# Performance work log

Hardware: AMD Instinct MI355X
Metric: run time of the kernel (lower is better)

The kernel has to match this reference:

```python
import jax, jax.numpy as jnp
import numpy as np

NEG_SLOPE = 0.2  # neg_slope init kwarg


def _segment_softmax(logits, seg, n):
    # numerically stable softmax over edges grouped by destination node
    m = jax.ops.segment_max(logits, seg, num_segments=n)          # [N,H]
    e = jnp.exp(logits - m[seg])                                   # [E,H]
    s = jax.ops.segment_sum(e, seg, num_segments=n)                # [N,H]
    return e / (s[seg] + 1e-16)


def _gat_conv(x, src, dst, W, att_src, att_dst, b, n):
    # PyG GATConv (add_self_loops already applied to src/dst), dropout off (eval)
    H, C = att_src.shape
    h = (x @ W).reshape(n, H, C)                                   # [N,H,C]
    a_src = jnp.einsum('nhc,hc->nh', h, att_src)                   # [N,H]
    a_dst = jnp.einsum('nhc,hc->nh', h, att_dst)                   # [N,H]
    logits = jax.nn.leaky_relu(a_src[src] + a_dst[dst], NEG_SLOPE)  # [E,H]
    alpha = _segment_softmax(logits, dst, n)                       # [E,H]
    msg = h[src] * alpha[:, :, None]                               # [E,H,C]
    out = jax.ops.segment_sum(msg, dst, num_segments=n)            # [N,H,C]
    return out.reshape(n, H * C) + b


def setup_inputs() -> dict:
    key = jax.random.key(0)
    ks = jax.random.split(key, 11)
    NU, NI = 10000, 100000
    N = NU + NI
    E = 1_000_000
    IN, HID, HEADS, OUT = 64, 64, 4, 64
    s = 0.1
    return {
        'edge_index': jax.random.randint(ks[0], (2, E), 0, N, dtype=jnp.int64)
            if jax.config.jax_enable_x64 else jax.random.randint(ks[0], (2, E), 0, N),
        'emb_user': jax.random.normal(ks[1], (NU, IN), jnp.float32) * s,
        'emb_item': jax.random.normal(ks[2], (NI, IN), jnp.float32) * s,
        'W1': jax.random.normal(ks[3], (IN, HEADS * HID), jnp.float32) * s,
        'att_src1': jax.random.normal(ks[4], (HEADS, HID), jnp.float32) * s,
        'att_dst1': jax.random.normal(ks[5], (HEADS, HID), jnp.float32) * s,
        'b1': jnp.zeros((HEADS * HID,), jnp.float32),
        'W2': jax.random.normal(ks[6], (HEADS * HID, OUT), jnp.float32) * s,
        'att_src2': jax.random.normal(ks[7], (1, OUT), jnp.float32) * s,
        'att_dst2': jax.random.normal(ks[8], (1, OUT), jnp.float32) * s,
        'b2': jnp.zeros((OUT,), jnp.float32),
    }


def reference(edge_index, emb_user, emb_item, W1, att_src1, att_dst1, b1,
              W2, att_src2, att_dst2, b2):
    NU = emb_user.shape[0]
    N = NU + emb_item.shape[0]
    x = jnp.concatenate([emb_user, emb_item], axis=0)              # [N,IN]
    # GATConv adds self-loops by default
    loops = jnp.arange(N, dtype=edge_index.dtype)
    src = jnp.concatenate([edge_index[0], loops])
    dst = jnp.concatenate([edge_index[1], loops])
    # dropout layers are identity in eval mode
    x = _gat_conv(x, src, dst, W1, att_src1, att_dst1, b1, N)      # [N,HEADS*HID]
    x = jax.nn.elu(x)
    x = _gat_conv(x, src, dst, W2, att_src2, att_dst2, b2, N)      # [N,OUT]
    return x[:NU], x[NU:]
```

## Files before the change

### kernel.cpp

```cpp
#include <hip/hip_runtime.h>
#include <math.h>


typedef float f32x4 __attribute__((ext_vector_type(4)));
typedef short s16x8 __attribute__((ext_vector_type(8)));

#define CHUNK 2048
#define CAPB 6400
#define PADM 1536
#define CAPT (CAPB + PADM)
#define G2PAD 264
#define SMASK 131071

static __device__ __forceinline__ short f2bf(float f) {
    unsigned u = __builtin_bit_cast(unsigned, f);
    u = (u + 0x7fff + ((u >> 16) & 1)) >> 16;
    return (short)u;
}
static __device__ __forceinline__ float bf2f(unsigned short u) {
    unsigned v = ((unsigned)u) << 16;
    return __builtin_bit_cast(float, v);
}


__global__ __launch_bounds__(256) void bin_kernel(
    const int* __restrict__ ei, int E, int ET, int* __restrict__ acur,
    unsigned long long* __restrict__ staging) {
    __shared__ int cnt[256], delta[256], cur[256];
    int t = threadIdx.x;
    cnt[t] = 0;
    __syncthreads();
    int c0 = blockIdx.x * CHUNK;
    int cend = min(c0 + CHUNK, ET);
    for (int e = c0 + t; e < cend; e += 256) {
        int d = (e < E) ? ei[E + e] : (e - E);
        atomicAdd(&cnt[d >> 9], 1);
    }
    __syncthreads();
    if (t < 64) {
        int loc[4], run = 0;
#pragma unroll
        for (int j = 0; j < 4; ++j) { int v = cnt[t * 4 + j]; loc[j] = run; run += v; }
        int inc = run;
#pragma unroll
        for (int off = 1; off < 64; off <<= 1) {
            int u = __shfl_up(inc, off);
            if (t >= off) inc += u;
        }
        int excl = inc - run;
#pragma unroll
        for (int j = 0; j < 4; ++j) {
            int b = t * 4 + j;
            int lofs = excl + loc[j];
            int c = cnt[b];
            int g = (c > 0) ? atomicAdd(&acur[b], c) : 0;
            delta[b] = b * CAPB + g - lofs;
            cur[b] = lofs;
        }
    }
    __syncthreads();
    for (int e = c0 + t; e < cend; e += 256) {
        int s, d;
        if (e < E) { s = ei[e]; d = ei[E + e]; } else { s = e - E; d = e - E; }
        unsigned long long v = ((unsigned long long)(unsigned)d << 32) | (unsigned)s;
        int b = d >> 9;
        int p = atomicAdd(&cur[b], 1);
        int idx = delta[b] + p;
        if (idx < (b + 1) * CAPB) staging[idx] = v;
    }
}

__global__ __launch_bounds__(256) void bucket_scan_kernel(
    const int* __restrict__ acur, int* __restrict__ bbase, int NB) {
    __shared__ int sc[256];
    int t = threadIdx.x;
    int v = 0;
    if (t < NB) {
        int c = min(acur[t], CAPB);
        v = ((c + 3) & ~3) + PADM;
    }
    sc[t] = v;
    __syncthreads();
    if (t == 0) {
        int run = 0;
        for (int i = 0; i < NB; ++i) { int x = sc[i]; sc[i] = run; run += x; }
    }
    __syncthreads();
    if (t < NB) bbase[t] = sc[t];
}

__global__ __launch_bounds__(256) void bucket_build_kernel(
    const unsigned long long* __restrict__ staging, const int* __restrict__ acur,
    const int* __restrict__ bbase, const float* __restrict__ as1e,
    const float* __restrict__ ad1e, int* __restrict__ offs, int* __restrict__ ends,
    int* __restrict__ csr, int* __restrict__ dstA, float* __restrict__ wts1T,
    int N, int ETp, int NB) {
    __shared__ int src_s[CAPT];
    __shared__ unsigned short ln_s[CAPT];
    __shared__ float adl[512 * 8];
    __shared__ int cnt[512];
    __shared__ int lofs[512];
    __shared__ int tot4_s;
    int b = blockIdx.x;
    int t = threadIdx.x;
    int n0 = b << 9;
    int nn = min(512, N - n0);
    int tot = min(acur[b], CAPB);
    for (int i = t; i < nn * 8; i += 256) adl[i] = ad1e[(size_t)n0 * 8 + i];
    for (int i = t; i < 512; i += 256) cnt[i] = 0;
    for (int i = t; i < CAPT; i += 256) src_s[i] = -1;
    __syncthreads();
    const unsigned long long* sp = staging + (size_t)b * CAPB;
    for (int i = t; i < tot; i += 256)
        atomicAdd(&cnt[(int)(sp[i] >> 32) - n0], 1);
    __syncthreads();
    if (t < 64) {
        int loc[8];
        int run = 0;
#pragma unroll
        for (int j = 0; j < 8; ++j) {
            int v = (cnt[t * 8 + j] + 3) & ~3;
            loc[j] = run;
            run += v;
        }
        int inc = run;
#pragma unroll
        for (int off = 1; off < 64; off <<= 1) {
            int u = __shfl_up(inc, off);
            if (t >= off) inc += u;
        }
        int excl = inc - run;
#pragma unroll
        for (int j = 0; j < 8; ++j) lofs[t * 8 + j] = excl + loc[j];
        if (t == 63) tot4_s = inc;
    }
    __syncthreads();
    int base = bbase[b];
    int tot4 = tot4_s;
    for (int i = t; i < nn; i += 256) {
        int beg = base + lofs[i];
        offs[n0 + i] = beg;
        ends[n0 + i] = beg + ((cnt[i] + 3) & ~3);
    }
    if (b == NB - 1 && t == 0) offs[N] = base + tot4;
    __syncthreads();
    for (int i = t; i < 512; i += 256) cnt[i] = 0;
    __syncthreads();
    for (int i = t; i < tot; i += 256) {
        unsigned long long v = sp[i];
        int s = (int)(v & 0xffffffffu);
        int ln = (int)(v >> 32) - n0;
        int p = lofs[ln] + atomicAdd(&cnt[ln], 1);
        src_s[p] = s;
        ln_s[p] = (unsigned short)ln;
    }
    __syncthreads();
    for (int i = t; i < tot4; i += 256) {
        int s = src_s[i];
        if (s < 0) {
            csr[base + i] = 0;
            dstA[base + i] = -1;
            wts1T[(size_t)0 * ETp + base + i] = 0.f;
            wts1T[(size_t)1 * ETp + base + i] = 0.f;
            wts1T[(size_t)2 * ETp + base + i] = 0.f;
            wts1T[(size_t)3 * ETp + base + i] = 0.f;
        } else {
            int ln = ln_s[i];
            csr[base + i] = s;
            dstA[base + i] = n0 + ln;
            const float4* ap = reinterpret_cast<const float4*>(as1e + (size_t)s * 8);
            float4 a0 = ap[0], a1 = ap[1];
            const float* dl = adl + ln * 8;
            float wA, wB;
            wA = a0.x * dl[0]; wB = a0.y * dl[1];
            wts1T[(size_t)0 * ETp + base + i] = (wA >= 1.f) ? wA : wB;
            wA = a0.z * dl[2]; wB = a0.w * dl[3];
            wts1T[(size_t)1 * ETp + base + i] = (wA >= 1.f) ? wA : wB;
            wA = a1.x * dl[4]; wB = a1.y * dl[5];
            wts1T[(size_t)2 * ETp + base + i] = (wA >= 1.f) ? wA : wB;
            wA = a1.z * dl[6]; wB = a1.w * dl[7];
            wts1T[(size_t)3 * ETp + base + i] = (wA >= 1.f) ? wA : wB;
        }
    }
}

__global__ void edge_w2_kernel(const int* __restrict__ csr,
                               const int* __restrict__ dstA,
                               const float* __restrict__ as2e,
                               const float* __restrict__ ad2e,
                               float* __restrict__ wts2, int ETp, int N) {
    int p = blockIdx.x * blockDim.x + threadIdx.x;
    if (p >= ETp) return;
    int d = dstA[p];
    int s = csr[p];
    if ((unsigned)d >= (unsigned)N || (unsigned)s >= (unsigned)N) {
        wts2[p] = 0.f;
        return;
    }
    float2 ae = *reinterpret_cast<const float2*>(as2e + (size_t)s * 2);
    float2 de = *reinterpret_cast<const float2*>(ad2e + (size_t)d * 2);
    float wA = ae.x * de.x, wB = ae.y * de.y;
    wts2[p] = (wA >= 1.f) ? wA : wB;
}

__global__ void prep_attv_kernel(const float* __restrict__ W1,
                                 const float* __restrict__ attS1,
                                 const float* __restrict__ attD1,
                                 const float* __restrict__ W2,
                                 const float* __restrict__ attS2,
                                 const float* __restrict__ attD2,
                                 float* __restrict__ attv1s, float* __restrict__ attv1d,
                                 float* __restrict__ attv2s, float* __restrict__ attv2d) {
    int t = threadIdx.x;
    {
        int k = t >> 2, h = t & 3;
        float ss = 0.f, sd = 0.f;
        for (int c = 0; c < 64; ++c) {
            float w = W1[k * 256 + h * 64 + c];
            ss += w * attS1[h * 64 + c];
            sd += w * attD1[h * 64 + c];
        }
        attv1s[k * 4 + h] = ss;
        attv1d[k * 4 + h] = sd;
    }
    {
        float ss = 0.f, sd = 0.f;
        for (int c = 0; c < 64; ++c) {
            float w = W2[t * 64 + c];
            ss += w * attS2[c];
            sd += w * attD2[c];
        }
        attv2s[t] = ss;
        attv2d[t] = sd;
    }
}

__global__ __launch_bounds__(256) void cast_att_kernel(
    const float* __restrict__ xu, const float* __restrict__ xi, int NU, int N,
    const float* __restrict__ attv1s, const float* __restrict__ attv1d,
    unsigned short* __restrict__ xb, float* __restrict__ as1e,
    float* __restrict__ ad1e) {
    int t = threadIdx.x;
    int wv = t >> 6, l = t & 63, l15 = l & 15, lg = l >> 4;

    s16x8 Bfr[2];
#pragma unroll
    for (int ks = 0; ks < 2; ++ks) {
        s16x8 f;
#pragma unroll
        for (int j = 0; j < 8; ++j) {
            int k = ks * 32 + lg * 8 + j;
            float v = 0.f;
            if (l15 < 4) v = attv1s[k * 4 + l15];
            else if (l15 < 8) v = attv1d[k * 4 + (l15 - 4)];
            f[j] = f2bf(v);
        }
        Bfr[ks] = f;
    }

    int ntile = (N + 15) >> 4;
    int wid = blockIdx.x * 4 + wv;
    int stride = gridDim.x * 4;
    for (int tile = wid; tile < ntile; tile += stride) {
        int rbase = tile * 16;
        int arow = rbase + l15;
        bool valid = (arow < N);
        if (!valid) arow = N - 1;
        const float* xp = (arow < NU) ? (xu + (size_t)arow * 64)
                                      : (xi + (size_t)(arow - NU) * 64);
        s16x8 Afr[2];
#pragma unroll
        for (int ks = 0; ks < 2; ++ks) {
            const float4* p = reinterpret_cast<const float4*>(xp + ks * 32 + lg * 8);
            float4 v0 = p[0];
            float4 v1 = p[1];
            s16x8 f;
            f[0] = f2bf(v0.x); f[1] = f2bf(v0.y); f[2] = f2bf(v0.z); f[3] = f2bf(v0.w);
            f[4] = f2bf(v1.x); f[5] = f2bf(v1.y); f[6] = f2bf(v1.z); f[7] = f2bf(v1.w);
            Afr[ks] = f;
            if (valid)
                *reinterpret_cast<s16x8*>(xb + (size_t)arow * 64 + ks * 32 + lg * 8) = f;
        }
        f32x4 acc = (f32x4){0.f, 0.f, 0.f, 0.f};
        acc = __builtin_amdgcn_mfma_f32_16x16x32_bf16(Afr[0], Bfr[0], acc, 0, 0, 0);
        acc = __builtin_amdgcn_mfma_f32_16x16x32_bf16(Afr[1], Bfr[1], acc, 0, 0, 0);
        if (l15 < 8) {
            float* dst = (l15 < 4) ? as1e : ad1e;
            int h = l15 & 3;
#pragma unroll
            for (int i = 0; i < 4; ++i) {
                int r = rbase + lg * 4 + i;
                if (r < N) {
                    float s = acc[i];
                    dst[(size_t)r * 8 + h * 2 + 0] = __expf(s);
                    dst[(size_t)r * 8 + h * 2 + 1] = __expf(0.2f * s);
                }
            }
        }
    }
}

__global__ __launch_bounds__(256) void agg1_kernel(
    const unsigned short* __restrict__ xb, const float* __restrict__ wts1T,
    const int* __restrict__ offs, const int* __restrict__ ends,
    const int* __restrict__ csr, unsigned short* __restrict__ yb, int N, int ETp) {
    int wv = threadIdx.x >> 6, lane = threadIdx.x & 63;
    int n = __builtin_amdgcn_readfirstlane(blockIdx.x * 4 + wv);
    if (n >= N) return;
    int h = lane >> 4, c4 = (lane & 15) * 4;
    int beg = offs[n], end = ends[n];
    const float* wp = wts1T + (size_t)h * ETp;
    float ss = 0.f, a0 = 0.f, a1 = 0.f, a2 = 0.f, a3 = 0.f;

    f32x4 w0, w1, w2;
    ushort4 r0[4], r1[4], r2[4];

#define A1_LOAD(W, R, O)                                                          \
    {                                                                             \
        W = *reinterpret_cast<const f32x4*>(wp + (O));                            \
        _Pragma("unroll") for (int j = 0; j < 4; ++j) {                           \
            int sj = __builtin_amdgcn_readfirstlane(csr[(O) + j]) & SMASK;        \
            R[j] = *reinterpret_cast<const ushort4*>(xb + (size_t)sj * 64 + c4);  \
        }                                                                         \
    }
#define A1_PROC(W, R)                                                            \
    {                                                                            \
        _Pragma("unroll") for (int j = 0; j < 4; ++j) {                          \
            float w = W[j];                                                      \
            ss += w;                                                             \
            a0 += w * bf2f(R[j].x);                                             \
            a1 += w * bf2f(R[j].y);                                             \
            a2 += w * bf2f(R[j].z);                                             \
            a3 += w * bf2f(R[j].w);                                             \
        }                                                                        \
    }

    A1_LOAD(w0, r0, beg)
    A1_LOAD(w1, r1, beg + 4)
    int o = beg;
    while (true) {
        if (o + 8 < end) A1_LOAD(w2, r2, o + 8)
        A1_PROC(w0, r0)
        o += 4; if (o >= end) break;
        if (o + 8 < end) A1_LOAD(w0, r0, o + 8)
        A1_PROC(w1, r1)
        o += 4; if (o >= end) break;
        if (o + 8 < end) A1_LOAD(w1, r1, o + 8)
        A1_PROC(w2, r2)
        o += 4; if (o >= end) break;
    }
#undef A1_LOAD
#undef A1_PROC
    float inv = 1.f / (ss + 1e-16f);
    ushort4 ov;
    ov.x = (unsigned short)f2bf(a0 * inv);
    ov.y = (unsigned short)f2bf(a1 * inv);
    ov.z = (unsigned short)f2bf(a2 * inv);
    ov.w = (unsigned short)f2bf(a3 * inv);
    *reinterpret_cast<ushort4*>(yb + (size_t)n * 256 + h * 64 + c4) = ov;
}

__global__ __launch_bounds__(256) void gemm_mid_mfma(
    const unsigned short* __restrict__ yb, int N, const float* __restrict__ W1,
    const float* __restrict__ b1, const float* __restrict__ attv2s,
    const float* __restrict__ attv2d, unsigned short* __restrict__ x2,
    float* __restrict__ as2e, float* __restrict__ ad2e) {
    __shared__ float part_s[16][4];
    __shared__ float part_d[16][4];
    int t = threadIdx.x;
    int wv = t >> 6;
    int l = t & 63;
    int l15 = l & 15;
    int lg = l >> 4;

    s16x8 Bfr[4][2];
#pragma unroll
    for (int c = 0; c < 4; ++c)
#pragma unroll
        for (int ks = 0; ks < 2; ++ks) {
            s16x8 f;
#pragma unroll
            for (int j = 0; j < 8; ++j)
                f[j] = f2bf(W1[(size_t)(ks * 32 + lg * 8 + j) * 256 + (wv * 4 + c) * 16 + l15]);
            Bfr[c][ks] = f;
        }
    float bv[4], avs[4], avd[4];
#pragma unroll
    for (int c = 0; c < 4; ++c) {
        int col = (wv * 4 + c) * 16 + l15;
        bv[c] = b1[col];
        avs[c] = attv2s[col];
        avd[c] = attv2d[col];
    }

    int ntile = (N + 15) >> 4;
    for (int tile = blockIdx.x; tile < ntile; tile += gridDim.x) {
        int rbase = tile * 16;
        int arow = rbase + l15;
        if (arow >= N) arow = N - 1;
        const unsigned short* yp = yb + (size_t)arow * 256 + wv * 64;
        s16x8 Afr0 = *reinterpret_cast<const s16x8*>(yp + lg * 8);
        s16x8 Afr1 = *reinterpret_cast<const s16x8*>(yp + 32 + lg * 8);
        f32x4 acc[4];
#pragma unroll
        for (int c = 0; c < 4; ++c) acc[c] = (f32x4){0.f, 0.f, 0.f, 0.f};
#pragma unroll
        for (int c = 0; c < 4; ++c) {
            acc[c] = __builtin_amdgcn_mfma_f32_16x16x32_bf16(Afr0, Bfr[c][0], acc[c], 0, 0, 0);
            acc[c] = __builtin_amdgcn_mfma_f32_16x16x32_bf16(Afr1, Bfr[c][1], acc[c], 0, 0, 0);
        }
        int r0 = rbase + lg * 4;
        float rs[4] = {0.f, 0.f, 0.f, 0.f};
        float rd[4] = {0.f, 0.f, 0.f, 0.f};
#pragma unroll
        for (int c = 0; c < 4; ++c) {
            int col = (wv * 4 + c) * 16 + l15;
#pragma unroll
            for (int i = 0; i < 4; ++i) {
                float v = acc[c][i] + bv[c];
                v = (v > 0.f) ? v : __expf(v) - 1.f;
                rs[i] += v * avs[c];
                rd[i] += v * avd[c];
                int r = r0 + i;
                if (r < N)
                    x2[(size_t)r * 256 + col] = (unsigned short)f2bf(v);
            }
        }
#pragma unroll
        for (int i = 0; i < 4; ++i) {
#pragma unroll
            for (int msk = 8; msk; msk >>= 1) {
                rs[i] += __shfl_xor(rs[i], msk);
                rd[i] += __shfl_xor(rd[i], msk);
            }
            if (l15 == 0) {
                part_s[lg * 4 + i][wv] = rs[i];
                part_d[lg * 4 + i][wv] = rd[i];
            }
        }
        __syncthreads();
        if (t < 16) {
            int r = rbase + t;
            if (r < N) {
                float s = part_s[t][0] + part_s[t][1] + part_s[t][2] + part_s[t][3];
                float d = part_d[t][0] + part_d[t][1] + part_d[t][2] + part_d[t][3];
                as2e[(size_t)r * 2 + 0] = __expf(s);
                as2e[(size_t)r * 2 + 1] = __expf(0.2f * s);
                ad2e[(size_t)r * 2 + 0] = __expf(d);
                ad2e[(size_t)r * 2 + 1] = __expf(0.2f * d);
            }
        }
        __syncthreads();
    }
}

__global__ __launch_bounds__(256) void gemm2_mfma(
    const unsigned short* __restrict__ x2, int N, const float* __restrict__ W2,
    unsigned short* __restrict__ h2) {
    __shared__ unsigned short at[16 * G2PAD];
    int t = threadIdx.x;
    int wv = t >> 6;
    int l = t & 63;
    int l15 = l & 15;
    int lg = l >> 4;

    s16x8 Bfr[8];
#pragma unroll
    for (int ks = 0; ks < 8; ++ks) {
        s16x8 f;
#pragma unroll
        for (int j = 0; j < 8; ++j)
            f[j] = f2bf(W2[(size_t)(ks * 32 + lg * 8 + j) * 64 + wv * 16 + l15]);
        Bfr[ks] = f;
    }

    int ntile = (N + 15) >> 4;
    for (int tile = blockIdx.x; tile < ntile; tile += gridDim.x) {
        int rbase = tile * 16;
        __syncthreads();
#pragma unroll
        for (int k = 0; k < 2; ++k) {
            int i = t * 2 + k;
            int row = i >> 5, c8 = i & 31;
            int r = rbase + row;
            if (r >= N) r = N - 1;
            *reinterpret_cast<uint4*>(at + row * G2PAD + c8 * 8) =
                *reinterpret_cast<const uint4*>(x2 + (size_t)r * 256 + c8 * 8);
        }
        __syncthreads();
        f32x4 acc = (f32x4){0.f, 0.f, 0.f, 0.f};
#pragma unroll
        for (int ks = 0; ks < 8; ++ks) {
            s16x8 Afr = *reinterpret_cast<const s16x8*>(at + l15 * G2PAD + ks * 32 + lg * 8);
            acc = __builtin_amdgcn_mfma_f32_16x16x32_bf16(Afr, Bfr[ks], acc, 0, 0, 0);
        }
        int r0 = rbase + lg * 4;
#pragma unroll
        for (int i = 0; i < 4; ++i) {
            int r = r0 + i;
            if (r < N)
                h2[(size_t)r * 64 + wv * 16 + l15] = (unsigned short)f2bf(acc[i]);
        }
    }
}

__global__ __launch_bounds__(256) void agg2_kernel(
    const unsigned short* __restrict__ h2, const float* __restrict__ wts2,
    const int* __restrict__ offs, const int* __restrict__ ends,
    const int* __restrict__ csr, const float* __restrict__ b2,
    float* __restrict__ out, int N) {
    int wv = threadIdx.x >> 6, lane = threadIdx.x & 63;
    int n = __builtin_amdgcn_readfirstlane(blockIdx.x * 4 + wv);
    if (n >= N) return;
    int beg = offs[n], end = ends[n];
    float ss = 0.f, acc = 0.f;

    f32x4 w0, w1, w2;
    unsigned short r0[4], r1[4], r2[4];

#define A2_LOAD(W, R, O)                                                   \
    {                                                                      \
        W = *reinterpret_cast<const f32x4*>(wts2 + (O));                   \
        _Pragma("unroll") for (int j = 0; j < 4; ++j) {                    \
            int sj = __builtin_amdgcn_readfirstlane(csr[(O) + j]) & SMASK; \
            R[j] = h2[(size_t)sj * 64 + lane];                             \
        }                                                                  \
    }
#define A2_PROC(W, R)                                                      \
    {                                                                      \
        _Pragma("unroll") for (int j = 0; j < 4; ++j) {                    \
            float w = W[j];                                                \
            ss += w;                                                       \
            acc += w * bf2f(R[j]);                                         \
        }                                                                  \
    }

    A2_LOAD(w0, r0, beg)
    A2_LOAD(w1, r1, beg + 4)
    int o = beg;
    while (true) {
        if (o + 8 < end) A2_LOAD(w2, r2, o + 8)
        A2_PROC(w0, r0)
        o += 4; if (o >= end) break;
        if (o + 8 < end) A2_LOAD(w0, r0, o + 8)
        A2_PROC(w1, r1)
        o += 4; if (o >= end) break;
        if (o + 8 < end) A2_LOAD(w1, r1, o + 8)
        A2_PROC(w2, r2)
        o += 4; if (o >= end) break;
    }
#undef A2_LOAD
#undef A2_PROC
    out[(size_t)n * 64 + lane] = acc / (ss + 1e-16f) + b2[lane];
}


extern "C" void kernel_launch(void* const* d_in, const int* in_sizes, int n_in,
                              void* d_out, int out_size, void* d_ws, size_t ws_size,
                              hipStream_t stream) {
    const int* ei = (const int*)d_in[0];
    const float* xu = (const float*)d_in[1];
    const float* xi = (const float*)d_in[2];
    const float* W1 = (const float*)d_in[3];
    const float* attS1 = (const float*)d_in[4];
    const float* attD1 = (const float*)d_in[5];
    const float* b1 = (const float*)d_in[6];
    const float* W2 = (const float*)d_in[7];
    const float* attS2 = (const float*)d_in[8];
    const float* attD2 = (const float*)d_in[9];
    const float* b2 = (const float*)d_in[10];
    float* out = (float*)d_out;

    const int E = in_sizes[0] / 2;
    const int NU = in_sizes[1] / 64;
    const int NI = in_sizes[2] / 64;
    const int N = NU + NI;
    const int ET = E + N;
    const int NB = (N + 511) >> 9;
    const int ETp = NB * CAPT;

    char* p = (char*)d_ws;
    auto carve = [&](size_t bytes) {
        void* r = (void*)p;
        p += (bytes + 255) & ~(size_t)255;
        return r;
    };
    unsigned short* xb = (unsigned short*)carve((size_t)N * 64 * 2);
    unsigned short* yb = (unsigned short*)carve((size_t)N * 256 * 2);
    unsigned short* x2 = (unsigned short*)carve((size_t)N * 256 * 2);
    float* as1e = (float*)carve((size_t)N * 8 * 4);
    float* ad1e = (float*)carve((size_t)N * 8 * 4);
    float* as2e = (float*)carve((size_t)N * 2 * 4);
    float* ad2e = (float*)carve((size_t)N * 2 * 4);
    float* attv1s = (float*)carve(256 * 4);
    float* attv1d = (float*)carve(256 * 4);
    float* attv2s = (float*)carve(256 * 4);
    float* attv2d = (float*)carve(256 * 4);
    int* offs = (int*)carve((size_t)(N + 1) * 4);
    int* ends = (int*)carve((size_t)N * 4);
    int* csr = (int*)carve((size_t)ETp * 4);
    int* dstA = (int*)carve((size_t)ETp * 4);
    float* wts1T = (float*)carve((size_t)4 * ETp * 4);
    float* wts2 = (float*)carve(((size_t)ETp + 16) * 4);
    int* acur = (int*)carve((size_t)NB * 4);
    int* bbase = (int*)carve((size_t)NB * 4);
    unsigned long long* staging = (unsigned long long*)yb;
    unsigned short* h2 = yb;

    prep_attv_kernel<<<1, 256, 0, stream>>>(W1, attS1, attD1, W2, attS2, attD2,
                                            attv1s, attv1d, attv2s, attv2d);
    {
        int ntile = (N + 15) >> 4;
        cast_att_kernel<<<(ntile + 3) / 4, 256, 0, stream>>>(
            xu, xi, NU, N, attv1s, attv1d, xb, as1e, ad1e);
    }

    hipMemsetAsync(acur, 0, (size_t)NB * 4, stream);
    {
        int grid = (ET + CHUNK - 1) / CHUNK;
        bin_kernel<<<grid, 256, 0, stream>>>(ei, E, ET, acur, staging);
    }
    bucket_scan_kernel<<<1, 256, 0, stream>>>(acur, bbase, NB);
    bucket_build_kernel<<<NB, 256, 0, stream>>>(staging, acur, bbase, as1e, ad1e,
                                                offs, ends, csr, dstA, wts1T,
                                                N, ETp, NB);

    agg1_kernel<<<(N + 3) / 4, 256, 0, stream>>>(xb, wts1T, offs, ends, csr, yb, N, ETp);
    gemm_mid_mfma<<<1024, 256, 0, stream>>>(yb, N, W1, b1, attv2s, attv2d, x2, as2e, ad2e);

    {
        int grid = (ETp + 255) / 256;
        edge_w2_kernel<<<grid, 256, 0, stream>>>(csr, dstA, as2e, ad2e, wts2, ETp, N);
    }
    gemm2_mfma<<<1024, 256, 0, stream>>>(x2, N, W2, h2);
    agg2_kernel<<<(N + 3) / 4, 256, 0, stream>>>(h2, wts2, offs, ends, csr, b2, out, N);
}
```

Baseline: 243.3 us.

## Cache edges in LDS during binning; preload CSR indices via shuffle in aggregations

The binning kernel now processes 4096 edges per block and keeps the packed (dst,src) pairs in shared memory after the counting pass, so the scatter pass no longer re-reads the edge index from global memory. In both aggregation kernels, nodes with at most 64 neighbours load their whole CSR segment with one coalesced per-lane load and broadcast indices with wave shuffles, replacing per-edge scalar loads. This aims to cut redundant global traffic and dependent load latency, at the cost of 32KB of LDS per bin block, fewer bin blocks, and a duplicated code path.

```diff
diff --git a/kernel.cpp b/kernel.cpp
--- a/kernel.cpp
+++ b/kernel.cpp
@@ -5,7 +5,7 @@
 typedef float f32x4 __attribute__((ext_vector_type(4)));
 typedef short s16x8 __attribute__((ext_vector_type(8)));
 
-#define CHUNK 2048
+#define CHUNK 4096
 #define CAPB 6400
 #define PADM 1536
 #define CAPT (CAPB + PADM)
@@ -26,15 +26,23 @@
 __global__ __launch_bounds__(256) void bin_kernel(
     const int* __restrict__ ei, int E, int ET, int* __restrict__ acur,
     unsigned long long* __restrict__ staging) {
+    __shared__ unsigned long long eds[CHUNK];
     __shared__ int cnt[256], delta[256], cur[256];
     int t = threadIdx.x;
     cnt[t] = 0;
     __syncthreads();
     int c0 = blockIdx.x * CHUNK;
-    int cend = min(c0 + CHUNK, ET);
-    for (int e = c0 + t; e < cend; e += 256) {
-        int d = (e < E) ? ei[E + e] : (e - E);
-        atomicAdd(&cnt[d >> 9], 1);
+#pragma unroll
+    for (int i = t; i < CHUNK; i += 256) {
+        int e = c0 + i;
+        unsigned long long v = ~0ull;
+        if (e < ET) {
+            int s, d;
+            if (e < E) { s = ei[e]; d = ei[E + e]; } else { s = e - E; d = e - E; }
+            v = ((unsigned long long)(unsigned)d << 32) | (unsigned)s;
+            atomicAdd(&cnt[d >> 9], 1);
+        }
+        eds[i] = v;
     }
     __syncthreads();
     if (t < 64) {
@@ -59,11 +67,10 @@
         }
     }
     __syncthreads();
-    for (int e = c0 + t; e < cend; e += 256) {
-        int s, d;
-        if (e < E) { s = ei[e]; d = ei[E + e]; } else { s = e - E; d = e - E; }
-        unsigned long long v = ((unsigned long long)(unsigned)d << 32) | (unsigned)s;
-        int b = d >> 9;
+    for (int i = t; i < CHUNK; i += 256) {
+        unsigned long long v = eds[i];
+        if (v == ~0ull) continue;
+        int b = (int)(v >> 32) >> 9;
         int p = atomicAdd(&cur[b], 1);
         int idx = delta[b] + p;
         if (idx < (b + 1) * CAPB) staging[idx] = v;
@@ -315,6 +322,50 @@
     f32x4 w0, w1, w2;
     ushort4 r0[4], r1[4], r2[4];
 
+    if (end - beg <= 64) {
+        int ci = beg + lane;
+        if (ci >= end) ci = beg;
+        int csrv = csr[ci] & SMASK;
+
+#define A1F_LOAD(W, R, O)                                                         \
+    {                                                                             \
+        W = *reinterpret_cast<const f32x4*>(wp + (O));                            \
+        _Pragma("unroll") for (int j = 0; j < 4; ++j) {                           \
+            int sj = __shfl(csrv, (O) - beg + j);                                 \
+            R[j] = *reinterpret_cast<const ushort4*>(xb + (size_t)sj * 64 + c4);  \
+        }                                                                         \
+    }
+#define A1_PROC(W, R)                                                            \
+    {                                                                            \
+        _Pragma("unroll") for (int j = 0; j < 4; ++j) {                          \
+            float w = W[j];                                                      \
+            ss += w;                                                             \
+            a0 += w * bf2f(R[j].x);                                              \
+            a1 += w * bf2f(R[j].y);                                              \
+            a2 += w * bf2f(R[j].z);                                              \
+            a3 += w * bf2f(R[j].w);                                              \
+        }                                                                        \
+    }
+        A1F_LOAD(w0, r0, beg)
+        if (beg + 4 < end) {
+            A1F_LOAD(w1, r1, beg + 4)
+            int o = beg;
+            while (true) {
+                if (o + 8 < end) A1F_LOAD(w2, r2, o + 8)
+                A1_PROC(w0, r0)
+                o += 4; if (o >= end) break;
+                if (o + 8 < end) A1F_LOAD(w0, r0, o + 8)
+                A1_PROC(w1, r1)
+                o += 4; if (o >= end) break;
+                if (o + 8 < end) A1F_LOAD(w1, r1, o + 8)
+                A1_PROC(w2, r2)
+                o += 4; if (o >= end) break;
+            }
+        } else {
+            A1_PROC(w0, r0)
+        }
+#undef A1F_LOAD
+    } else {
 #define A1_LOAD(W, R, O)                                                          \
     {                                                                             \
         W = *reinterpret_cast<const f32x4*>(wp + (O));                            \
@@ -323,34 +374,23 @@
             R[j] = *reinterpret_cast<const ushort4*>(xb + (size_t)sj * 64 + c4);  \
         }                                                                         \
     }
-#define A1_PROC(W, R)                                                            \
-    {                                                                            \
-        _Pragma("unroll") for (int j = 0; j < 4; ++j) {                          \
-            float w = W[j];                                                      \
-            ss += w;                                                             \
-            a0 += w * bf2f(R[j].x);                                             \
-            a1 += w * bf2f(R[j].y);                                             \
-            a2 += w * bf2f(R[j].z);                                             \
-            a3 += w * bf2f(R[j].w);                                             \
-        }                                                                        \
-    }
-
-    A1_LOAD(w0, r0, beg)
-    A1_LOAD(w1, r1, beg + 4)
-    int o = beg;
-    while (true) {
-        if (o + 8 < end) A1_LOAD(w2, r2, o + 8)
-        A1_PROC(w0, r0)
-        o += 4; if (o >= end) break;
-        if (o + 8 < end) A1_LOAD(w0, r0, o + 8)
-        A1_PROC(w1, r1)
-        o += 4; if (o >= end) break;
-        if (o + 8 < end) A1_LOAD(w1, r1, o + 8)
-        A1_PROC(w2, r2)
-        o += 4; if (o >= end) break;
-    }
+        A1_LOAD(w0, r0, beg)
+        A1_LOAD(w1, r1, beg + 4)
+        int o = beg;
+        while (true) {
+            if (o + 8 < end) A1_LOAD(w2, r2, o + 8)
+            A1_PROC(w0, r0)
+            o += 4; if (o >= end) break;
+            if (o + 8 < end) A1_LOAD(w0, r0, o + 8)
+            A1_PROC(w1, r1)
+            o += 4; if (o >= end) break;
+            if (o + 8 < end) A1_LOAD(w1, r1, o + 8)
+            A1_PROC(w2, r2)
+            o += 4; if (o >= end) break;
+        }
 #undef A1_LOAD
 #undef A1_PROC
+    }
     float inv = 1.f / (ss + 1e-16f);
     ushort4 ov;
     ov.x = (unsigned short)f2bf(a0 * inv);
@@ -518,6 +558,47 @@
     f32x4 w0, w1, w2;
     unsigned short r0[4], r1[4], r2[4];
 
+    if (end - beg <= 64) {
+        int ci = beg + lane;
+        if (ci >= end) ci = beg;
+        int csrv = csr[ci] & SMASK;
+
+#define A2F_LOAD(W, R, O)                                                  \
+    {                                                                      \
+        W = *reinterpret_cast<const f32x4*>(wts2 + (O));                   \
+        _Pragma("unroll") for (int j = 0; j < 4; ++j) {                    \
+            int sj = __shfl(csrv, (O) - beg + j);                          \
+            R[j] = h2[(size_t)sj * 64 + lane];                             \
+        }                                                                  \
+    }
+#define A2_PROC(W, R)                                                      \
+    {                                                                      \
+        _Pragma("unroll") for (int j = 0; j < 4; ++j) {                    \
+            float w = W[j];                                                \
+            ss += w;                                                       \
+            acc += w * bf2f(R[j]);                                         \
+        }                                                                  \
+    }
+        A2F_LOAD(w0, r0, beg)
+        if (beg + 4 < end) {
+            A2F_LOAD(w1, r1, beg + 4)
+            int o = beg;
+            while (true) {
+                if (o + 8 < end) A2F_LOAD(w2, r2, o + 8)
+                A2_PROC(w0, r0)
+                o += 4; if (o >= end) break;
+                if (o + 8 < end) A2F_LOAD(w0, r0, o + 8)
+                A2_PROC(w1, r1)
+                o += 4; if (o >= end) break;
+                if (o + 8 < end) A2F_LOAD(w1, r1, o + 8)
+                A2_PROC(w2, r2)
+                o += 4; if (o >= end) break;
+            }
+        } else {
+            A2_PROC(w0, r0)
+        }
+#undef A2F_LOAD
+    } else {
 #define A2_LOAD(W, R, O)                                                   \
     {                                                                      \
         W = *reinterpret_cast<const f32x4*>(wts2 + (O));                   \
@@ -526,31 +607,23 @@
             R[j] = h2[(size_t)sj * 64 + lane];                             \
         }                                                                  \
     }
-#define A2_PROC(W, R)                                                      \
-    {                                                                      \
-        _Pragma("unroll") for (int j = 0; j < 4; ++j) {                    \
-            float w = W[j];                                                \
-            ss += w;                                                       \
-            acc += w * bf2f(R[j]);                                         \
-        }                                                                  \
-    }
-
-    A2_LOAD(w0, r0, beg)
-    A2_LOAD(w1, r1, beg + 4)
-    int o = beg;
-    while (true) {
-        if (o + 8 < end) A2_LOAD(w2, r2, o + 8)
-        A2_PROC(w0, r0)
-        o += 4; if (o >= end) break;
-        if (o + 8 < end) A2_LOAD(w0, r0, o + 8)
-        A2_PROC(w1, r1)
-        o += 4; if (o >= end) break;
-        if (o + 8 < end) A2_LOAD(w1, r1, o + 8)
-        A2_PROC(w2, r2)
-        o += 4; if (o >= end) break;
-    }
+        A2_LOAD(w0, r0, beg)
+        A2_LOAD(w1, r1, beg + 4)
+        int o = beg;
+        while (true) {
+            if (o + 8 < end) A2_LOAD(w2, r2, o + 8)
+            A2_PROC(w0, r0)
+            o += 4; if (o >= end) break;
+            if (o + 8 < end) A2_LOAD(w0, r0, o + 8)
+            A2_PROC(w1, r1)
+            o += 4; if (o >= end) break;
+            if (o + 8 < end) A2_LOAD(w1, r1, o + 8)
+            A2_PROC(w2, r2)
+            o += 4; if (o >= end) break;
+        }
 #undef A2_LOAD
 #undef A2_PROC
+    }
     out[(size_t)n * 64 + lane] = acc / (ss + 1e-16f) + b2[lane];
 }
 
```

New measurement: 232.8 us (median of 2 runs). -4.3%, faster.
